# Kernel tuning notes

Measured on AMD Instinct MI355X. Metric: run time of the kernel, lower is better.

The kernel has to match this reference:

```python
import jax, jax.numpy as jnp
import numpy as np

N = 20000
E = 320000
IN_DIM = 16
H = 128
HEADS = 4
NEG_SLOPE = 0.2  # GATv2Conv default
EPS_LN = 1e-5


def setup_inputs() -> dict:
    key = jax.random.key(0)
    ks = jax.random.split(key, 16)
    f32 = jnp.float32
    def rn(k, shape, scale):
        return jax.random.normal(k, shape, dtype=f32) * scale
    s_in = 1.0 / np.sqrt(IN_DIM)
    s_h = 1.0 / np.sqrt(H)
    s_4h = 1.0 / np.sqrt(4 * H)
    s_2h = 1.0 / np.sqrt(2 * H)
    inp = {}
    inp["x"] = jax.random.normal(ks[0], (N, IN_DIM), dtype=f32)
    inp["edge_index"] = jax.random.randint(ks[1], (2, E), 0, N)
    inp["edge_attr"] = jax.random.normal(ks[2], (E, 2), dtype=f32)
    inp["emb_w"] = rn(ks[3], (IN_DIM, H), s_in)
    inp["emb_b"] = jnp.zeros((H,), f32)
    # 3 GATv2 layers stacked on leading axis
    inp["lin_l"] = rn(ks[4], (3, H, HEADS * H), s_h)
    inp["lin_r"] = rn(ks[5], (3, H, HEADS * H), s_h)
    inp["lin_edge"] = rn(ks[6], (3, 2, HEADS * H), 1.0 / np.sqrt(2.0))
    inp["att"] = rn(ks[7], (3, HEADS, H), s_h)
    inp["conv_bias01"] = jnp.zeros((2, HEADS * H), f32)  # concat=True layers
    inp["conv_bias2"] = jnp.zeros((H,), f32)             # concat=False layer
    inp["proj_w"] = rn(ks[8], (2, HEADS * H, H), s_4h)
    inp["proj_b"] = jnp.zeros((2, H), f32)
    inp["n1_g"] = jnp.ones((3, H), f32)
    inp["n1_b"] = jnp.zeros((3, H), f32)
    inp["n2_g"] = jnp.ones((3, H), f32)
    inp["n2_b"] = jnp.zeros((3, H), f32)
    inp["ffn_w1"] = rn(ks[9], (3, H, 2 * H), s_h)
    inp["ffn_b1"] = jnp.zeros((3, 2 * H), f32)
    inp["ffn_w2"] = rn(ks[10], (3, 2 * H, H), s_2h)
    inp["ffn_b2"] = jnp.zeros((3, H), f32)
    return inp


def layer_norm(x, g, b):
    mu = jnp.mean(x, axis=-1, keepdims=True)
    var = jnp.mean((x - mu) ** 2, axis=-1, keepdims=True)
    return (x - mu) * jax.lax.rsqrt(var + EPS_LN) * g + b


def gatv2(h, src, dst, eattr, Wl, Wr, We, att, bias, concat, n):
    # h: [n, H]; per-edge gather -> GATv2 attention -> segment softmax -> scatter-add
    xl = (h @ Wl).reshape(n, HEADS, H)   # source transform
    xr = (h @ Wr).reshape(n, HEADS, H)   # target transform
    ee = (eattr @ We).reshape(-1, HEADS, H)
    e = jax.nn.leaky_relu(xl[src] + xr[dst] + ee, NEG_SLOPE)  # [E', HEADS, H]
    score = jnp.einsum('ehc,hc->eh', e, att)                  # [E', HEADS]
    smax = jax.ops.segment_max(score, dst, num_segments=n)
    p = jnp.exp(score - smax[dst])
    denom = jax.ops.segment_sum(p, dst, num_segments=n)
    alpha = p / (denom[dst] + 1e-16)
    out = jax.ops.segment_sum(xl[src] * alpha[..., None], dst, num_segments=n)
    if concat:
        return out.reshape(n, HEADS * H) + bias
    return jnp.mean(out, axis=1) + bias


def reference(x, edge_index, edge_attr, emb_w, emb_b, lin_l, lin_r, lin_edge, att,
              conv_bias01, conv_bias2, proj_w, proj_b, n1_g, n1_b, n2_g, n2_b,
              ffn_w1, ffn_b1, ffn_w2, ffn_b2):
    n = x.shape[0]
    e = edge_attr.shape[0]
    # PyG add_self_loops with fill_value='mean': self-loop attr = mean of incoming edge attrs
    ones = jnp.ones((e,), x.dtype)
    deg = jax.ops.segment_sum(ones, edge_index[1], num_segments=n)
    loop_attr = jax.ops.segment_sum(edge_attr, edge_index[1], num_segments=n) / jnp.maximum(deg, 1.0)[:, None]
    ar = jnp.arange(n)
    src = jnp.concatenate([edge_index[0], ar])
    dst = jnp.concatenate([edge_index[1], ar])
    ea = jnp.concatenate([edge_attr, loop_attr], axis=0)

    h = x @ emb_w + emb_b
    for i in range(3):
        concat = i < 2
        bias = conv_bias01[i] if concat else conv_bias2
        h_in = h
        h = gatv2(h, src, dst, ea, lin_l[i], lin_r[i], lin_edge[i], att[i], bias, concat, n)
        if concat:
            h = h @ proj_w[i] + proj_b[i]
        h = layer_norm(h + h_in, n1_g[i], n1_b[i])
        h2 = h
        h = jax.nn.gelu(h @ ffn_w1[i] + ffn_b1[i], approximate=False) @ ffn_w2[i] + ffn_b2[i]
        h = layer_norm(h + h2, n2_g[i], n2_b[i])
    return h
```

## Files before the change

kernel.cpp:

```cpp
#include <hip/hip_runtime.h>
#include <math.h>

#define IN_DIM 16
#define HDIM   128
#define HEADS  4
#define HH     512
#define FFH    256
#define NEG_SLOPE 0.2f

typedef _Float16 half8 __attribute__((ext_vector_type(8)));
typedef _Float16 h8 __attribute__((ext_vector_type(8)));
typedef _Float16 h4 __attribute__((ext_vector_type(4)));
typedef _Float16 h2 __attribute__((ext_vector_type(2)));
typedef float f32x4 __attribute__((ext_vector_type(4)));

struct __align__(8) Edge { int src; _Float16 ea0, ea1; };

static __device__ inline float hsum8(h8 v) {
    h4 a = __builtin_shufflevector(v, v, 0, 1, 2, 3) +
           __builtin_shufflevector(v, v, 4, 5, 6, 7);
    h2 b = __builtin_shufflevector(a, a, 0, 1) +
           __builtin_shufflevector(a, a, 2, 3);
    return (float)b[0] + (float)b[1];
}

__global__ void xpad_kernel(const float* __restrict__ x, _Float16* __restrict__ xh, int n) {
    int idx = blockIdx.x * 256 + threadIdx.x;
    if (idx >= n * 64) return;
    int r = idx >> 6, k = idx & 63;
    xh[idx] = (k < IN_DIM) ? (_Float16)x[r * IN_DIM + k] : (_Float16)0.0f;
}

struct WDesc { const float* src; _Float16* dst; int Ksrc; int lgKd; int lgN; };
struct WDescs { WDesc d[15]; };
__global__ void wconv_kernel(WDescs ds) {
    WDesc w = ds.d[blockIdx.y];
    int Kd = 1 << w.lgKd;
    int total = 1 << (w.lgKd + w.lgN);
    for (int idx = blockIdx.x * 256 + threadIdx.x; idx < total; idx += gridDim.x * 256) {
        int n2 = idx >> w.lgKd, k = idx & (Kd - 1);
        w.dst[idx] = (k < w.Ksrc) ? (_Float16)w.src[(k << w.lgN) + n2] : (_Float16)0.0f;
    }
}

__global__ void deg_kernel(const int* __restrict__ ei, const float* __restrict__ eattr,
                           float* deg, float* asum, int E) {
    int e = blockIdx.x * blockDim.x + threadIdx.x;
    if (e >= E) return;
    int d = ei[E + e];
    atomicAdd(&deg[d], 1.0f);
    atomicAdd(&asum[2 * d], eattr[2 * e]);
    atomicAdd(&asum[2 * d + 1], eattr[2 * e + 1]);
}

__global__ void scan_kernel(const float* __restrict__ deg, int* row_ptr, int* cur, int n) {
    __shared__ int sums[1024];
    int tid = threadIdx.x;
    int per = (n + 1023) / 1024;
    int s0 = tid * per;
    int s1 = s0 + per; if (s1 > n) s1 = n;
    int s = 0;
    for (int i = s0; i < s1; i++) s += (int)deg[i] + 1;
    int mysum = s;
    sums[tid] = s;
    __syncthreads();
    for (int dd = 1; dd < 1024; dd <<= 1) {
        int t = (tid >= dd) ? sums[tid - dd] : 0;
        __syncthreads();
        sums[tid] += t;
        __syncthreads();
    }
    int run = sums[tid] - mysum;
    for (int i = s0; i < s1; i++) {
        row_ptr[i] = run; cur[i] = run;
        run += (int)deg[i] + 1;
    }
    if (tid == 1023) row_ptr[n] = sums[1023];
}

__global__ void scatter_kernel(const int* __restrict__ ei, const float* __restrict__ eattr,
                               const float* __restrict__ deg, const float* __restrict__ asum,
                               int* cur, Edge* csr, int E, int n) {
    int i = blockIdx.x * blockDim.x + threadIdx.x;
    if (i >= E + n) return;
    Edge ed;
    int pos;
    if (i < E) {
        int d = ei[E + i];
        pos = atomicAdd(&cur[d], 1);
        ed.src = ei[i];
        ed.ea0 = (_Float16)eattr[2 * i];
        ed.ea1 = (_Float16)eattr[2 * i + 1];
    } else {
        int nd = i - E;
        float dv = fmaxf(deg[nd], 1.0f);
        pos = atomicAdd(&cur[nd], 1);
        ed.src = nd;
        ed.ea0 = (_Float16)(asum[2 * nd] / dv);
        ed.ea1 = (_Float16)(asum[2 * nd + 1] / dv);
    }
    csr[pos] = ed;
}

template <int OUTMODE, int BM>
__global__ __launch_bounds__(256) void gemm_mfma(const _Float16* __restrict__ A, int lda,
                                                 const _Float16* __restrict__ BT,
                                                 const float* __restrict__ bias,
                                                 float* __restrict__ C32,
                                                 _Float16* __restrict__ C16,
                                                 int M, int N, int K) {
    const int BK = 64, PAD = 8, NI = BM / 32;
    __shared__ _Float16 As[BM][BK + PAD];
    __shared__ _Float16 Bs[128][BK + PAD];
    int tid = threadIdx.x;
    int wave = tid >> 6, lane = tid & 63;
    int quad = lane >> 4, l16 = lane & 15;
    int wrow = (wave >> 1) * (16 * NI);
    int wcol = (wave & 1) * 64;
    int mBase = blockIdx.y * BM;
    int n0 = blockIdx.x * 128;

    f32x4 acc[NI][4] = {};

    for (int k0 = 0; k0 < K; k0 += BK) {
#pragma unroll
        for (int t = 0; t < BM / 32; t++) {
            int idx = tid + t * 256;
            int r = idx >> 3, kb = (idx & 7) * 8;
            half8 hv = {};
            int grow = mBase + r;
            if (grow < M) hv = *(const half8*)(A + (size_t)grow * lda + k0 + kb);
            *(half8*)&As[r][kb] = hv;
        }
#pragma unroll
        for (int t = 0; t < 4; t++) {
            int idx = tid + t * 256;
            int r = idx >> 3, kb = (idx & 7) * 8;
            *(half8*)&Bs[r][kb] = *(const half8*)(BT + (size_t)(n0 + r) * K + k0 + kb);
        }
        __syncthreads();
#pragma unroll
        for (int kc = 0; kc < 2; kc++) {
            half8 a[NI], b[4];
#pragma unroll
            for (int i = 0; i < NI; i++)
                a[i] = *(const half8*)&As[wrow + i * 16 + l16][kc * 32 + quad * 8];
#pragma unroll
            for (int j = 0; j < 4; j++)
                b[j] = *(const half8*)&Bs[wcol + j * 16 + l16][kc * 32 + quad * 8];
#pragma unroll
            for (int i = 0; i < NI; i++)
#pragma unroll
                for (int j = 0; j < 4; j++)
                    acc[i][j] = __builtin_amdgcn_mfma_f32_16x16x32_f16(a[i], b[j], acc[i][j], 0, 0, 0);
        }
        __syncthreads();
    }

#pragma unroll
    for (int i = 0; i < NI; i++) {
#pragma unroll
        for (int r = 0; r < 4; r++) {
            int row = mBase + wrow + i * 16 + quad * 4 + r;
            if (row >= M) continue;
#pragma unroll
            for (int j = 0; j < 4; j++) {
                int col = n0 + wcol + j * 16 + l16;
                float v = acc[i][j][r] + (bias ? bias[col] : 0.0f);
                if (OUTMODE == 0 || OUTMODE == 2)
                    C32[(size_t)row * N + col] = v;
                if (OUTMODE == 1 || OUTMODE == 2)
                    C16[(size_t)row * N + col] = (_Float16)v;
            }
        }
    }
}

__global__ __launch_bounds__(256) void gemm_ln(const _Float16* __restrict__ A, int lda,
                                               const _Float16* __restrict__ BT,
                                               const float* __restrict__ bias,
                                               const float* __restrict__ R,
                                               const float* __restrict__ g,
                                               const float* __restrict__ b,
                                               float* __restrict__ C32,
                                               _Float16* __restrict__ C16,
                                               int M, int K) {
    const int BK = 64, PAD = 8;
    __shared__ _Float16 As[64][BK + PAD];
    __shared__ _Float16 Bs[128][BK + PAD];
    int tid = threadIdx.x;
    int wave = tid >> 6, lane = tid & 63;
    int quad = lane >> 4, l16 = lane & 15;
    int mBase = blockIdx.x * 64;

    f32x4 acc[8] = {};

    for (int k0 = 0; k0 < K; k0 += BK) {
#pragma unroll
        for (int t = 0; t < 2; t++) {
            int idx = tid + t * 256;
            int r = idx >> 3, kb = (idx & 7) * 8;
            half8 hv = {};
            int grow = mBase + r;
            if (grow < M) hv = *(const half8*)(A + (size_t)grow * lda + k0 + kb);
            *(half8*)&As[r][kb] = hv;
        }
#pragma unroll
        for (int t = 0; t < 4; t++) {
            int idx = tid + t * 256;
            int r = idx >> 3, kb = (idx & 7) * 8;
            *(half8*)&Bs[r][kb] = *(const half8*)(BT + (size_t)r * K + k0 + kb);
        }
        __syncthreads();
#pragma unroll
        for (int kc = 0; kc < 2; kc++) {
            half8 a = *(const half8*)&As[wave * 16 + l16][kc * 32 + quad * 8];
#pragma unroll
            for (int j = 0; j < 8; j++) {
                half8 bb = *(const half8*)&Bs[j * 16 + l16][kc * 32 + quad * 8];
                acc[j] = __builtin_amdgcn_mfma_f32_16x16x32_f16(a, bb, acc[j], 0, 0, 0);
            }
        }
        __syncthreads();
    }

    float gj[8], bj[8], biasj[8];
#pragma unroll
    for (int j = 0; j < 8; j++) {
        int col = j * 16 + l16;
        biasj[j] = bias[col];
        gj[j] = g[col];
        bj[j] = b[col];
    }
    int row0 = mBase + wave * 16 + quad * 4;
    float sum[4] = {}, sq[4] = {};
#pragma unroll
    for (int r = 0; r < 4; r++) {
        int row = row0 + r;
        bool ok = row < M;
        size_t base = (size_t)row * HDIM;
#pragma unroll
        for (int j = 0; j < 8; j++) {
            float v = acc[j][r] + biasj[j] + (ok ? R[base + j * 16 + l16] : 0.0f);
            acc[j][r] = v;
            sum[r] += v;
            sq[r] += v * v;
        }
    }
#pragma unroll
    for (int r = 0; r < 4; r++) {
#pragma unroll
        for (int off = 1; off < 16; off <<= 1) {
            sum[r] += __shfl_xor(sum[r], off);
            sq[r] += __shfl_xor(sq[r], off);
        }
    }
#pragma unroll
    for (int r = 0; r < 4; r++) {
        int row = row0 + r;
        if (row >= M) continue;
        size_t base = (size_t)row * HDIM;
        float mu = sum[r] * (1.0f / HDIM);
        float var = sq[r] * (1.0f / HDIM) - mu * mu;
        float invstd = rsqrtf(var + 1e-5f);
#pragma unroll
        for (int j = 0; j < 8; j++) {
            float o = (acc[j][r] - mu) * invstd * gj[j] + bj[j];
            C32[base + j * 16 + l16] = o;
            if (C16) C16[base + j * 16 + l16] = (_Float16)o;
        }
    }
}

__global__ __launch_bounds__(256) void ffn_fused(const _Float16* __restrict__ A,
                                                 const _Float16* __restrict__ W1T,
                                                 const float* __restrict__ b1,
                                                 const _Float16* __restrict__ W2T,
                                                 const float* __restrict__ b2,
                                                 const float* __restrict__ R,
                                                 const float* __restrict__ g,
                                                 const float* __restrict__ b,
                                                 float* __restrict__ C32,
                                                 _Float16* __restrict__ C16,
                                                 int M) {
    __shared__ _Float16 Ws[128][128 + 8];
    __shared__ _Float16 Mid[64][256 + 8];
    int tid = threadIdx.x;
    int wave = tid >> 6, lane = tid & 63;
    int quad = lane >> 4, l16 = lane & 15;
    int mBase = blockIdx.x * 64;

    half8 afrag[4];
    {
        int row = mBase + wave * 16 + l16;
#pragma unroll
        for (int kc = 0; kc < 4; kc++) {
            if (row < M)
                afrag[kc] = *(const half8*)(A + (size_t)row * HDIM + kc * 32 + quad * 8);
            else
                afrag[kc] = (half8)(_Float16)0.0f;
        }
    }

#pragma unroll
    for (int h = 0; h < 2; h++) {
        if (h) __syncthreads();
#pragma unroll
        for (int t = 0; t < 8; t++) {
            int idx = tid + t * 256;
            int r = idx >> 4, kb = (idx & 15) * 8;
            *(half8*)&Ws[r][kb] = *(const half8*)(W1T + (size_t)(h * 128 + r) * HDIM + kb);
        }
        __syncthreads();
        f32x4 acc[8] = {};
#pragma unroll
        for (int kc = 0; kc < 4; kc++) {
#pragma unroll
            for (int j = 0; j < 8; j++) {
                half8 bb = *(const half8*)&Ws[j * 16 + l16][kc * 32 + quad * 8];
                acc[j] = __builtin_amdgcn_mfma_f32_16x16x32_f16(afrag[kc], bb, acc[j], 0, 0, 0);
            }
        }
#pragma unroll
        for (int j = 0; j < 8; j++) {
            float bj1 = b1[h * 128 + j * 16 + l16];
#pragma unroll
            for (int r = 0; r < 4; r++) {
                float v = acc[j][r] + bj1;
                v = 0.5f * v * (1.0f + erff(v * 0.70710678118654752f));
                Mid[wave * 16 + quad * 4 + r][h * 128 + j * 16 + l16] = (_Float16)v;
            }
        }
    }
    __syncthreads();

    f32x4 acc2[8] = {};
#pragma unroll
    for (int kc2 = 0; kc2 < 2; kc2++) {
        if (kc2) __syncthreads();
#pragma unroll
        for (int t = 0; t < 8; t++) {
            int idx = tid + t * 256;
            int r = idx >> 4, kb = (idx & 15) * 8;
            *(half8*)&Ws[r][kb] = *(const half8*)(W2T + (size_t)r * FFH + kc2 * 128 + kb);
        }
        __syncthreads();
#pragma unroll
        for (int kc = 0; kc < 4; kc++) {
            half8 am = *(const half8*)&Mid[wave * 16 + l16][kc2 * 128 + kc * 32 + quad * 8];
#pragma unroll
            for (int j = 0; j < 8; j++) {
                half8 bb = *(const half8*)&Ws[j * 16 + l16][kc * 32 + quad * 8];
                acc2[j] = __builtin_amdgcn_mfma_f32_16x16x32_f16(am, bb, acc2[j], 0, 0, 0);
            }
        }
    }

    float gj[8], bj[8], b2j[8];
#pragma unroll
    for (int j = 0; j < 8; j++) {
        int col = j * 16 + l16;
        b2j[j] = b2[col];
        gj[j] = g[col];
        bj[j] = b[col];
    }
    int row0 = mBase + wave * 16 + quad * 4;
    float sum[4] = {}, sq[4] = {};
#pragma unroll
    for (int r = 0; r < 4; r++) {
        int row = row0 + r;
        bool ok = row < M;
        size_t base = (size_t)row * HDIM;
#pragma unroll
        for (int j = 0; j < 8; j++) {
            float v = acc2[j][r] + b2j[j] + (ok ? R[base + j * 16 + l16] : 0.0f);
            acc2[j][r] = v;
            sum[r] += v;
            sq[r] += v * v;
        }
    }
#pragma unroll
    for (int r = 0; r < 4; r++) {
#pragma unroll
        for (int off = 1; off < 16; off <<= 1) {
            sum[r] += __shfl_xor(sum[r], off);
            sq[r] += __shfl_xor(sq[r], off);
        }
    }
#pragma unroll
    for (int r = 0; r < 4; r++) {
        int row = row0 + r;
        if (row >= M) continue;
        size_t base = (size_t)row * HDIM;
        float mu = sum[r] * (1.0f / HDIM);
        float var = sq[r] * (1.0f / HDIM) - mu * mu;
        float invstd = rsqrtf(var + 1e-5f);
#pragma unroll
        for (int j = 0; j < 8; j++) {
            float o = (acc2[j][r] - mu) * invstd * gj[j] + bj[j];
            C32[base + j * 16 + l16] = o;
            if (C16) C16[base + j * 16 + l16] = (_Float16)o;
        }
    }
}

__global__ __launch_bounds__(256) void gat_edge_kernel(
    const _Float16* __restrict__ XLR,
    const int* __restrict__ row_ptr, const Edge* __restrict__ csr,
    const float* __restrict__ We,
    const float* __restrict__ attW,
    const float* __restrict__ cbias,
    _Float16* __restrict__ OUT16, float* __restrict__ OUT32,
    const float* __restrict__ R, const float* __restrict__ lng,
    const float* __restrict__ lnb, _Float16* __restrict__ OUT16h,
    int n, int concat) {
    int tid = threadIdx.x;
    int wave = tid >> 6, lane = tid & 63;
    int node = blockIdx.x * 4 + wave;
    if (node >= n) return;
    int c0 = lane * 8;

    h8 xr8 = *(const h8*)(XLR + (size_t)node * 1024 + 512 + c0);
    h8 w08, w18, att8;
#pragma unroll
    for (int k = 0; k < 8; k++) {
        w08[k] = (_Float16)We[c0 + k];
        w18[k] = (_Float16)We[HH + c0 + k];
        att8[k] = (_Float16)attW[c0 + k];
    }
    const _Float16 slope = (_Float16)NEG_SLOPE;

    h8 acc2 = (h8)(_Float16)0.0f;
    float m = -INFINITY, l = 0.0f;
    int beg = row_ptr[node], end = row_ptr[node + 1];
    int j = beg;
    for (; j + 1 < end; j += 2) {
        Edge e0 = csr[j], e1 = csr[j + 1];
        h8 x0 = *(const h8*)(XLR + (size_t)e0.src * 1024 + c0);
        h8 x1 = *(const h8*)(XLR + (size_t)e1.src * 1024 + c0);
        h8 v0 = x0 + (xr8 + w08 * e0.ea0 + w18 * e0.ea1);
        h8 v1 = x1 + (xr8 + w08 * e1.ea0 + w18 * e1.ea1);
        v0 = __builtin_elementwise_max(v0, v0 * slope);
        v1 = __builtin_elementwise_max(v1, v1 * slope);
        float p0 = hsum8(v0 * att8);
        float p1 = hsum8(v1 * att8);
        p0 += __shfl_xor(p0, 1); p1 += __shfl_xor(p1, 1);
        p0 += __shfl_xor(p0, 2); p1 += __shfl_xor(p1, 2);
        p0 += __shfl_xor(p0, 4); p1 += __shfl_xor(p1, 4);
        p0 += __shfl_xor(p0, 8); p1 += __shfl_xor(p1, 8);
        float mnew = fmaxf(m, fmaxf(p0, p1));
        float sc = __expf(m - mnew);
        float e0f = __expf(p0 - mnew);
        float e1f = __expf(p1 - mnew);
        l = l * sc + e0f + e1f;
        acc2 = acc2 * (_Float16)sc + x0 * (_Float16)e0f + x1 * (_Float16)e1f;
        m = mnew;
    }
    if (j < end) {
        Edge e0 = csr[j];
        h8 x0 = *(const h8*)(XLR + (size_t)e0.src * 1024 + c0);
        h8 v0 = x0 + (xr8 + w08 * e0.ea0 + w18 * e0.ea1);
        v0 = __builtin_elementwise_max(v0, v0 * slope);
        float p0 = hsum8(v0 * att8);
        p0 += __shfl_xor(p0, 1);
        p0 += __shfl_xor(p0, 2);
        p0 += __shfl_xor(p0, 4);
        p0 += __shfl_xor(p0, 8);
        float mnew = fmaxf(m, p0);
        float sc = __expf(m - mnew);
        float e0f = __expf(p0 - mnew);
        l = l * sc + e0f;
        acc2 = acc2 * (_Float16)sc + x0 * (_Float16)e0f;
        m = mnew;
    }
    float invf = 1.0f / (l + 1e-16f);
    if (concat) {
        h8 o = acc2 * (_Float16)invf;
#pragma unroll
        for (int k = 0; k < 8; k++) o[k] = o[k] + (_Float16)cbias[c0 + k];
        *(h8*)(OUT16 + (size_t)node * 1024 + c0) = o;
    } else {
        float o8[8];
#pragma unroll
        for (int k = 0; k < 8; k++) {
            float a = (float)acc2[k] * invf;
            a += __shfl_xor(a, 16);
            a += __shfl_xor(a, 32);
            o8[k] = a;
        }
        float v8[8];
        float sum = 0.0f, sq = 0.0f;
        if (lane < 16) {
#pragma unroll
            for (int k = 0; k < 8; k++) {
                float v = o8[k] * 0.25f + cbias[c0 + k] + R[(size_t)node * HDIM + c0 + k];
                v8[k] = v;
                sum += v;
                sq += v * v;
            }
        }
#pragma unroll
        for (int off = 1; off < 16; off <<= 1) {
            sum += __shfl_xor(sum, off);
            sq += __shfl_xor(sq, off);
        }
        if (lane < 16) {
            float mu = sum * (1.0f / HDIM);
            float var = sq * (1.0f / HDIM) - mu * mu;
            float invstd = rsqrtf(var + 1e-5f);
#pragma unroll
            for (int k = 0; k < 8; k++) {
                float o = (v8[k] - mu) * invstd * lng[c0 + k] + lnb[c0 + k];
                OUT32[(size_t)node * HDIM + c0 + k] = o;
                OUT16h[(size_t)node * HDIM + c0 + k] = (_Float16)o;
            }
        }
    }
}

extern "C" void kernel_launch(void* const* d_in, const int* in_sizes, int n_in,
                              void* d_out, int out_size, void* d_ws, size_t ws_size,
                              hipStream_t stream) {
    const float* x        = (const float*)d_in[0];
    const int*   ei       = (const int*)d_in[1];
    const float* eattr    = (const float*)d_in[2];
    const float* emb_w    = (const float*)d_in[3];
    const float* emb_b    = (const float*)d_in[4];
    const float* lin_l    = (const float*)d_in[5];
    const float* lin_r    = (const float*)d_in[6];
    const float* lin_edge = (const float*)d_in[7];
    const float* attw     = (const float*)d_in[8];
    const float* cb01     = (const float*)d_in[9];
    const float* cb2      = (const float*)d_in[10];
    const float* proj_w   = (const float*)d_in[11];
    const float* proj_b   = (const float*)d_in[12];
    const float* n1g      = (const float*)d_in[13];
    const float* n1b      = (const float*)d_in[14];
    const float* n2g      = (const float*)d_in[15];
    const float* n2b      = (const float*)d_in[16];
    const float* fw1      = (const float*)d_in[17];
    const float* fb1      = (const float*)d_in[18];
    const float* fw2      = (const float*)d_in[19];
    const float* fb2      = (const float*)d_in[20];
    float* out = (float*)d_out;

    const int n = in_sizes[0] / IN_DIM;
    const int E = in_sizes[2] / 2;
    const int EP = E + n;

    size_t off = 0;
    auto alloc = [&](size_t bytes) {
        void* p = (char*)d_ws + off;
        off += (bytes + 255) & ~(size_t)255;
        return p;
    };
    float* deg     = (float*)alloc((size_t)n * 4);
    float* asum    = (float*)alloc((size_t)2 * n * 4);
    int*   row_ptr = (int*)alloc((size_t)(n + 1) * 4);
    int*   cur     = (int*)alloc((size_t)n * 4);
    Edge*  csr     = (Edge*)alloc((size_t)EP * 8);
    float* H0      = (float*)alloc((size_t)n * HDIM * 4);
    float* H1      = (float*)alloc((size_t)n * HDIM * 4);
    _Float16* H0h  = (_Float16*)alloc((size_t)n * HDIM * 2);
    _Float16* H1h  = (_Float16*)alloc((size_t)n * HDIM * 2);
    _Float16* XLR  = (_Float16*)alloc((size_t)n * 1024 * 2);
    _Float16* xh   = (_Float16*)alloc((size_t)n * 64 * 2);
    _Float16* wt_emb  = (_Float16*)alloc((size_t)HDIM * 64 * 2);
    _Float16* wt_llr  = (_Float16*)alloc((size_t)3 * 1024 * HDIM * 2);
    _Float16* wt_proj = (_Float16*)alloc((size_t)2 * HDIM * HH * 2);
    _Float16* wt_f1   = (_Float16*)alloc((size_t)3 * FFH * HDIM * 2);
    _Float16* wt_f2   = (_Float16*)alloc((size_t)3 * HDIM * FFH * 2);
    (void)ws_size;

    xpad_kernel<<<(n * 64 + 255) / 256, 256, 0, stream>>>(x, xh, n);
    WDescs ds;
    int di = 0;
    ds.d[di++] = {emb_w, wt_emb, IN_DIM, 6, 7};
    for (int i = 0; i < 3; i++) {
        ds.d[di++] = {lin_l + (size_t)i * HDIM * HH, wt_llr + (size_t)i * 1024 * HDIM, HDIM, 7, 9};
        ds.d[di++] = {lin_r + (size_t)i * HDIM * HH, wt_llr + (size_t)i * 1024 * HDIM + (size_t)512 * HDIM, HDIM, 7, 9};
    }
    for (int i = 0; i < 2; i++)
        ds.d[di++] = {proj_w + (size_t)i * HH * HDIM, wt_proj + (size_t)i * HDIM * HH, HH, 9, 7};
    for (int i = 0; i < 3; i++)
        ds.d[di++] = {fw1 + (size_t)i * HDIM * FFH, wt_f1 + (size_t)i * FFH * HDIM, HDIM, 7, 8};
    for (int i = 0; i < 3; i++)
        ds.d[di++] = {fw2 + (size_t)i * FFH * HDIM, wt_f2 + (size_t)i * HDIM * FFH, FFH, 8, 7};
    wconv_kernel<<<dim3(32, 15), 256, 0, stream>>>(ds);

    (void)hipMemsetAsync(deg, 0, (size_t)n * 4, stream);
    (void)hipMemsetAsync(asum, 0, (size_t)2 * n * 4, stream);
    deg_kernel<<<(E + 255) / 256, 256, 0, stream>>>(ei, eattr, deg, asum, E);
    scan_kernel<<<1, 1024, 0, stream>>>(deg, row_ptr, cur, n);
    scatter_kernel<<<(EP + 255) / 256, 256, 0, stream>>>(ei, eattr, deg, asum, cur, csr, E, n);

    gemm_mfma<2, 128><<<dim3(1, (n + 127) / 128), 256, 0, stream>>>(
        xh, 64, wt_emb, emb_b, H0, H0h, n, HDIM, 64);

    for (int i = 0; i < 3; i++) {
        int concat = (i < 2);
        gemm_mfma<1, 128><<<dim3(8, (n + 127) / 128), 256, 0, stream>>>(
            H0h, HDIM, wt_llr + (size_t)i * 1024 * HDIM, nullptr, nullptr, XLR, n, 1024, HDIM);
        gat_edge_kernel<<<(n + 3) / 4, 256, 0, stream>>>(
            XLR, row_ptr, csr,
            lin_edge + (size_t)i * 2 * HH, attw + (size_t)i * HH,
            concat ? (cb01 + (size_t)i * HH) : cb2,
            XLR + 512, H1,
            H0, n1g + (size_t)i * HDIM, n1b + (size_t)i * HDIM, H1h,
            n, concat);
        if (concat) {
            gemm_ln<<<(n + 63) / 64, 256, 0, stream>>>(
                XLR + 512, 1024, wt_proj + (size_t)i * HDIM * HH,
                proj_b + (size_t)i * HDIM, H0,
                n1g + (size_t)i * HDIM, n1b + (size_t)i * HDIM,
                H1, H1h, n, HH);
        }
        float* lnout = (i == 2) ? out : H0;
        _Float16* lnout16 = (i == 2) ? nullptr : H0h;
        ffn_fused<<<(n + 63) / 64, 256, 0, stream>>>(
            H1h, wt_f1 + (size_t)i * FFH * HDIM, fb1 + (size_t)i * FFH,
            wt_f2 + (size_t)i * HDIM * FFH, fb2 + (size_t)i * HDIM, H1,
            n2g + (size_t)i * HDIM, n2b + (size_t)i * HDIM,
            lnout, lnout16, n);
    }
}
```

Measured before the change: 600.2 us.

## Keep B tile resident in registers and loop blocks over M tiles

Replaces the K-looped MFMA GEMM with a kernel that loads the whole 128-column weight slice (full K) into LDS once, pulls the B fragments into registers, and then iterates persistently over 64-row M tiles. A fragments are read directly from global memory with no LDS staging, and the main loop has no syncthreads. The XLR GEMM now uses a fixed grid of 8x80 blocks, which amortises the weight loads but gives fewer blocks and higher register pressure.

```diff
diff --git a/kernel.cpp b/kernel.cpp
--- a/kernel.cpp
+++ b/kernel.cpp
@@ -102,75 +102,74 @@
     csr[pos] = ed;
 }
 
-template <int OUTMODE, int BM>
-__global__ __launch_bounds__(256) void gemm_mfma(const _Float16* __restrict__ A, int lda,
-                                                 const _Float16* __restrict__ BT,
-                                                 const float* __restrict__ bias,
-                                                 float* __restrict__ C32,
-                                                 _Float16* __restrict__ C16,
-                                                 int M, int N, int K) {
-    const int BK = 64, PAD = 8, NI = BM / 32;
-    __shared__ _Float16 As[BM][BK + PAD];
-    __shared__ _Float16 Bs[128][BK + PAD];
+template <int KT, int OUTMODE>
+__global__ __launch_bounds__(256) void gemm_bstat(const _Float16* __restrict__ A, int lda,
+                                                  const _Float16* __restrict__ BT,
+                                                  const float* __restrict__ bias,
+                                                  float* __restrict__ C32,
+                                                  _Float16* __restrict__ C16,
+                                                  int M, int Nstride, int numMT) {
+    const int PAD = 8, KC = KT / 32;
+    __shared__ _Float16 Bs[128][KT + PAD];
     int tid = threadIdx.x;
     int wave = tid >> 6, lane = tid & 63;
     int quad = lane >> 4, l16 = lane & 15;
-    int wrow = (wave >> 1) * (16 * NI);
-    int wcol = (wave & 1) * 64;
-    int mBase = blockIdx.y * BM;
+    int wrow = (wave >> 1) * 32, wcol = (wave & 1) * 64;
     int n0 = blockIdx.x * 128;
 
-    f32x4 acc[NI][4] = {};
-
-    for (int k0 = 0; k0 < K; k0 += BK) {
-#pragma unroll
-        for (int t = 0; t < BM / 32; t++) {
-            int idx = tid + t * 256;
-            int r = idx >> 3, kb = (idx & 7) * 8;
-            half8 hv = {};
-            int grow = mBase + r;
-            if (grow < M) hv = *(const half8*)(A + (size_t)grow * lda + k0 + kb);
-            *(half8*)&As[r][kb] = hv;
-        }
-#pragma unroll
-        for (int t = 0; t < 4; t++) {
-            int idx = tid + t * 256;
-            int r = idx >> 3, kb = (idx & 7) * 8;
-            *(half8*)&Bs[r][kb] = *(const half8*)(BT + (size_t)(n0 + r) * K + k0 + kb);
-        }
-        __syncthreads();
-#pragma unroll
-        for (int kc = 0; kc < 2; kc++) {
-            half8 a[NI], b[4];
-#pragma unroll
-            for (int i = 0; i < NI; i++)
-                a[i] = *(const half8*)&As[wrow + i * 16 + l16][kc * 32 + quad * 8];
-#pragma unroll
-            for (int j = 0; j < 4; j++)
-                b[j] = *(const half8*)&Bs[wcol + j * 16 + l16][kc * 32 + quad * 8];
-#pragma unroll
-            for (int i = 0; i < NI; i++)
+#pragma unroll
+    for (int t = 0; t < KT / 16; t++) {
+        int idx = tid + t * 256;
+        int r = idx / (KT / 8), kb = (idx % (KT / 8)) * 8;
+        *(half8*)&Bs[r][kb] = *(const half8*)(BT + (size_t)(n0 + r) * KT + kb);
+    }
+    __syncthreads();
+
+    half8 bfrag[4][KC];
+#pragma unroll
+    for (int j = 0; j < 4; j++)
+#pragma unroll
+        for (int kc = 0; kc < KC; kc++)
+            bfrag[j][kc] = *(const half8*)&Bs[wcol + j * 16 + l16][kc * 32 + quad * 8];
+
+    float biasj[4];
+#pragma unroll
+    for (int j = 0; j < 4; j++)
+        biasj[j] = bias ? bias[n0 + wcol + j * 16 + l16] : 0.0f;
+
+    for (int mt = blockIdx.y; mt < numMT; mt += gridDim.y) {
+        int rbase = mt * 64 + wrow;
+        half8 af[2][KC];
+#pragma unroll
+        for (int i = 0; i < 2; i++) {
+            int row = rbase + i * 16 + l16;
+#pragma unroll
+            for (int kc = 0; kc < KC; kc++)
+                af[i][kc] = (row < M) ? *(const half8*)(A + (size_t)row * lda + kc * 32 + quad * 8)
+                                      : (half8)(_Float16)0.0f;
+        }
+        f32x4 acc[2][4] = {};
+#pragma unroll
+        for (int kc = 0; kc < KC; kc++)
+#pragma unroll
+            for (int i = 0; i < 2; i++)
 #pragma unroll
                 for (int j = 0; j < 4; j++)
-                    acc[i][j] = __builtin_amdgcn_mfma_f32_16x16x32_f16(a[i], b[j], acc[i][j], 0, 0, 0);
-        }
-        __syncthreads();
-    }
-
-#pragma unroll
-    for (int i = 0; i < NI; i++) {
-#pragma unroll
-        for (int r = 0; r < 4; r++) {
-            int row = mBase + wrow + i * 16 + quad * 4 + r;
-            if (row >= M) continue;
-#pragma unroll
-            for (int j = 0; j < 4; j++) {
-                int col = n0 + wcol + j * 16 + l16;
-                float v = acc[i][j][r] + (bias ? bias[col] : 0.0f);
-                if (OUTMODE == 0 || OUTMODE == 2)
-                    C32[(size_t)row * N + col] = v;
-                if (OUTMODE == 1 || OUTMODE == 2)
-                    C16[(size_t)row * N + col] = (_Float16)v;
+                    acc[i][j] = __builtin_amdgcn_mfma_f32_16x16x32_f16(af[i][kc], bfrag[j][kc], acc[i][j], 0, 0, 0);
+#pragma unroll
+        for (int i = 0; i < 2; i++) {
+#pragma unroll
+            for (int r = 0; r < 4; r++) {
+                int row = rbase + i * 16 + quad * 4 + r;
+                if (row >= M) continue;
+#pragma unroll
+                for (int j = 0; j < 4; j++) {
+                    int col = n0 + wcol + j * 16 + l16;
+                    float v = acc[i][j][r] + biasj[j];
+                    if (OUTMODE == 2)
+                        C32[(size_t)row * Nstride + col] = v;
+                    C16[(size_t)row * Nstride + col] = (_Float16)v;
+                }
             }
         }
     }
@@ -547,6 +546,7 @@
     const int n = in_sizes[0] / IN_DIM;
     const int E = in_sizes[2] / 2;
     const int EP = E + n;
+    const int numMT = (n + 63) / 64;
 
     size_t off = 0;
     auto alloc = [&](size_t bytes) {
@@ -594,13 +594,14 @@
     scan_kernel<<<1, 1024, 0, stream>>>(deg, row_ptr, cur, n);
     scatter_kernel<<<(EP + 255) / 256, 256, 0, stream>>>(ei, eattr, deg, asum, cur, csr, E, n);
 
-    gemm_mfma<2, 128><<<dim3(1, (n + 127) / 128), 256, 0, stream>>>(
-        xh, 64, wt_emb, emb_b, H0, H0h, n, HDIM, 64);
+    gemm_bstat<64, 2><<<dim3(1, numMT), 256, 0, stream>>>(
+        xh, 64, wt_emb, emb_b, H0, H0h, n, HDIM, numMT);
 
     for (int i = 0; i < 3; i++) {
         int concat = (i < 2);
-        gemm_mfma<1, 128><<<dim3(8, (n + 127) / 128), 256, 0, stream>>>(
-            H0h, HDIM, wt_llr + (size_t)i * 1024 * HDIM, nullptr, nullptr, XLR, n, 1024, HDIM);
+        gemm_bstat<128, 1><<<dim3(8, 80), 256, 0, stream>>>(
+            H0h, HDIM, wt_llr + (size_t)i * 1024 * HDIM, nullptr,
+            nullptr, XLR, n, 1024, numMT);
         gat_edge_kernel<<<(n + 3) / 4, 256, 0, stream>>>(
             XLR, row_ptr, csr,
             lin_edge + (size_t)i * 2 * HH, attw + (size_t)i * HH,
```

Result: faster. 568.7 us (-5.3%).
